# Optimization experiments

Hardware: AMD Instinct MI355X
Metric: run time of the kernel (lower is better)

## Reference

```python
import jax, jax.numpy as jnp
import numpy as np

B_, C_, T_, F_IN, H_, K_ = 64, 6, 128, 128, 128, 3


def _ln(x, g, b, eps=1e-5):
    # PyTorch LayerNorm: biased variance, eps=1e-5
    m = x.mean(-1, keepdims=True)
    v = ((x - m) ** 2).mean(-1, keepdims=True)
    return (x - m) / jnp.sqrt(v + eps) * g + b


def setup_inputs() -> dict:
    key = jax.random.key(0)
    ks = jax.random.split(key, 24)
    rn = lambda i, shape, s=1.0: jax.random.normal(ks[i], shape, jnp.float32) * s
    H = H_
    return dict(
        X_de=rn(0, (B_, C_, T_, F_IN)),
        # fe_proj: Linear(F_IN->H) + LayerNorm(H)
        W1=rn(1, (F_IN, H), 1.0 / np.sqrt(F_IN)), b1=rn(2, (H,), 0.02),
        ln1_g=1.0 + rn(3, (H,), 0.1), ln1_b=rn(4, (H,), 0.1),
        # LearnAdjacency: weight vector, scalar bias, LayerNorm(1)
        aw=rn(5, (H,), 0.1), ab=rn(6, (1,), 0.1),
        aln_g=1.0 + rn(7, (1,), 0.1), aln_b=rn(8, (1,), 0.1),
        # ChebConv: weights (K,H,H), bias (H), LayerNorm(H)
        cheb_w=rn(9, (K_, H, H), 1.0 / np.sqrt(H)), cheb_b=rn(10, (H,), 0.02),
        cln_g=1.0 + rn(11, (H,), 0.1), cln_b=rn(12, (H,), 0.1),
        # satt: Linear(2H->H) + LayerNorm(H) + Linear(H->1)
        sW1=rn(13, (2 * H, H), 1.0 / np.sqrt(2 * H)), sb1=rn(14, (H,), 0.02),
        sln_g=1.0 + rn(15, (H,), 0.1), sln_b=rn(16, (H,), 0.1),
        sW2=rn(17, (H, 1), 1.0 / np.sqrt(H)), sb2=rn(18, (1,), 0.02),
    )


def reference(X_de, W1, b1, ln1_g, ln1_b, aw, ab, aln_g, aln_b,
              cheb_w, cheb_b, cln_g, cln_b,
              sW1, sb1, sln_g, sln_b, sW2, sb2):
    b, C, T, Fin = X_de.shape
    H = W1.shape[1]
    K = cheb_w.shape[0]
    # fe_proj over every (b,t,c) node feature vector (Dropout = identity in eval)
    x = X_de.transpose(0, 2, 1, 3).reshape(b * T * C, Fin)  # (bTC, Fin)
    xn = jax.nn.gelu(_ln(x @ W1 + b1, ln1_g, ln1_b), approximate=False)
    Xn = xn.reshape(b, T, C, H)
    Xf = xn.reshape(b * T, C, H)  # fold T into batch; timesteps are independent
    # LearnAdjacency: pairwise |diff| -> scalar logit -> relu -> LayerNorm(1) -> row_softmax
    diff = jnp.abs(Xf[:, :, None, :] - Xf[:, None, :, :])  # (bT, C, C, H)
    logits = jax.nn.relu(jnp.einsum('bnjf,f->bnj', diff, aw) + ab)
    logits = _ln(logits[..., None], aln_g, aln_b)[..., 0]
    # row_softmax with eps=1e-8 in denominator (as in source)
    e = jnp.exp(logits - logits.max(-1, keepdims=True))
    adj = e / (e.sum(-1, keepdims=True) + 1e-8)  # (bT, C, C)
    # ChebConv with row-normalized A_hat = adj + I
    A_hat = adj + jnp.eye(C, dtype=adj.dtype)
    P = A_hat / jnp.maximum(A_hat.sum(-1, keepdims=True), 1e-6)
    out = jnp.einsum('bnf,fo->bno', Xf, cheb_w[0])
    Pk = Xf
    for k in range(1, K):  # K=3, static Chebyshev recurrence
        Pk = jnp.einsum('bnm,bmf->bnf', P, Pk)
        out = out + jnp.einsum('bnf,fo->bno', Pk, cheb_w[k])
    g = _ln(out + cheb_b, cln_g, cln_b)  # (bT, C, H); DropPath = identity in eval
    # attention gating
    nmean = jnp.einsum('bnm,bmf->bnf', adj, g)
    cat = jnp.concatenate([g, nmean], axis=-1)  # (bT, C, 2H)
    h = jax.nn.gelu(_ln(cat @ sW1 + sb1, sln_g, sln_b), approximate=False)
    att = jax.nn.sigmoid((h @ sW2 + sb2)[..., 0])[..., None]  # (bT, C, 1)
    epoch = (g * att).mean(axis=1)  # mean over nodes -> (bT, H)
    return (epoch.reshape(b, T, H),
            adj.reshape(b, T, C, C),
            Xn,
            g.reshape(b, T, C, H))
```

## Files before the change

### kernel.cpp

```cpp
#include <hip/hip_runtime.h>
#include <math.h>

typedef unsigned short u16;
typedef unsigned int u32;
typedef __attribute__((ext_vector_type(2))) float f32x2;
typedef __attribute__((ext_vector_type(4))) float f32x4;
typedef __attribute__((ext_vector_type(8))) short bf16x8;
typedef __attribute__((ext_vector_type(4))) u32 u32x4;

#define U_CONST   0.16666666638888889f
#define C1_CONST  0.5000000004166667f
#define C2_CONST  0.2500000004166667f
#define A_CONST   0.08333333326388889f
#define A1C_CONST 0.12499999993055555f

__device__ __forceinline__ float bf2f(u16 u){ union{u32 i; float f;} v; v.i=((u32)u)<<16; return v.f; }
__device__ __forceinline__ u16 f2bf(float f){ union{float f; u32 i;} v; v.f=f; u32 x=v.i;
  return (u16)((x + 0x7FFFu + ((x>>16)&1u)) >> 16); }

__device__ __forceinline__ u32 cvtpk(float lo, float hi){
  u32 r; asm("v_cvt_pk_bf16_f32 %0, %1, %2" : "=v"(r) : "v"(lo), "v"(hi)); return r;
}

__device__ __forceinline__ float gelu_f(float x){
  float ax = fabsf(x) * 0.7071067811865476f;
  float t  = __builtin_amdgcn_rcpf(fmaf(0.3275911f, ax, 1.0f));
  float p  = t*fmaf(t, fmaf(t, fmaf(t, fmaf(t, 1.061405429f, -1.453152027f),
                                    1.421413741f), -0.284496736f), 0.254829592f);
  float er = fmaf(-p, __expf(-ax*ax), 1.0f);
  er = copysignf(er, x);
  return 0.5f*x*(1.0f+er);
}
__device__ __forceinline__ float sigmoid_f(float z){
  return __builtin_amdgcn_rcpf(1.0f + __expf(-z));
}

__device__ __forceinline__ bf16x8 pack8(f32x4 a, f32x4 b){
  union { bf16x8 v; u32 w[4]; } r;
  r.w[0]=cvtpk(a[0],a[1]); r.w[1]=cvtpk(a[2],a[3]);
  r.w[2]=cvtpk(b[0],b[1]); r.w[3]=cvtpk(b[2],b[3]);
  return r.v;
}

template<bool GELU>
__device__ __forceinline__ void ln_rows(f32x4 (&acc)[8], const float* __restrict__ gvec,
                                        const float* __restrict__ bvec, int cl){
  float sm[4]={0,0,0,0}, sq[4]={0,0,0,0};
  #pragma unroll
  for (int n=0;n<8;n++)
    #pragma unroll
    for (int j=0;j<4;j++){ float x = acc[n][j]; sm[j]+=x; sq[j]+=x*x; }
  #pragma unroll
  for (int j=0;j<4;j++){
    #pragma unroll
    for (int off=1; off<16; off<<=1){ sm[j]+=__shfl_xor(sm[j],off); sq[j]+=__shfl_xor(sq[j],off); }
    float m = sm[j]*0.0078125f;
    float r = rsqrtf(sq[j]*0.0078125f - m*m + 1e-5f);
    sm[j]=m; sq[j]=r;
  }
  #pragma unroll
  for (int n=0;n<8;n++){
    float gg = gvec[(n<<4)+cl], be = bvec[(n<<4)+cl];
    #pragma unroll
    for (int j=0;j<4;j++){
      float y = (acc[n][j]-sm[j])*sq[j]*gg + be;
      acc[n][j] = GELU ? gelu_f(y) : y;
    }
  }
}

__device__ __forceinline__ void add_vec(f32x4 (&acc)[8], const float* __restrict__ v, int cl){
  #pragma unroll
  for (int n=0;n<8;n++){ float bv = v[(n<<4)+cl];
    #pragma unroll
    for (int j=0;j<4;j++) acc[n][j]+=bv; }
}

__device__ __forceinline__ void gsum(const f32x4 (&acc)[8], float (&s0)[8], float (&s1)[8], int cq){
  #pragma unroll
  for (int n=0;n<8;n++){
    float a=0.f, b=0.f;
    #pragma unroll
    for (int j=0;j<4;j++){
      int row = (cq<<2)+j;
      float y = acc[n][j];
      a += (row<6)? y : 0.f;
      b += (row>=6 && row<12)? y : 0.f;
    }
    a += __shfl_xor(a,16); a += __shfl_xor(a,32);
    b += __shfl_xor(b,16); b += __shfl_xor(b,32);
    s0[n]=a; s1[n]=b;
  }
}

__device__ __forceinline__ void spill(const f32x4 (&acc)[8], float* __restrict__ gdst,
                                      char* Al, int cl, int cq){
  #pragma unroll
  for (int n=0;n<8;n++)
    #pragma unroll
    for (int j=0;j<4;j++){
      int R=(cq<<2)+j;
      float y=acc[n][j], yo=__shfl_xor(y,1);
      if (R<12 && !(cl&1)){
        int col=(n<<4)+cl;
        *(f32x2*)(gdst + (size_t)R*128 + col) = (f32x2){y,yo};
        *(u32*)(Al + (R<<8) + ((col<<1) ^ ((R&7)<<4))) = cvtpk(y,yo);
      }
    }
}

__device__ __forceinline__ void ssave(const f32x4 (&acc)[8], char* Sl, int cl, int cq){
  float s0[8], s1[8];
  gsum(acc, s0, s1, cq);
  #pragma unroll
  for (int n=0;n<8;n++){
    float a_ = __shfl_xor(s0[n],1), b_ = __shfl_xor(s1[n],1);
    if (cq==0 && !(cl&1)){
      int col=(n<<4)+cl;
      *(u32*)(Sl + (col<<1))       = cvtpk(s0[n], a_);
      *(u32*)(Sl + 256 + (col<<1)) = cvtpk(s1[n], b_);
    }
  }
}

__device__ __forceinline__ void stageW(u16* Wb, const u16* __restrict__ slot, int tid){
  const u32x4* src = (const u32x4*)slot;
  #pragma unroll
  for (int it=0; it<4; ++it){
    int i = tid + (it<<9);
    int h = i >> 4, s = i & 15;
    u32x4 v = src[i];
    *(u32x4*)((char*)Wb + (h<<8) + ((s ^ (h&7))<<4)) = v;
  }
}
__device__ __forceinline__ bf16x8 bfrag(const u16* Wb, int col, int kt, int cq){
  int s = (kt<<2) + cq;
  return *(const bf16x8*)((const char*)Wb + (col<<8) + ((s ^ (col&7))<<4));
}
__device__ __forceinline__ bf16x8 afrag(const char* Al, int rl, int kt, int cq){
  return *(const bf16x8*)(Al + (rl<<8) + (((kt<<6)+(cq<<4)) ^ ((rl&7)<<4)));
}

template<bool INIT>
__device__ __forceinline__ void gemm_a(const u16* Wb, const char* Al, int rl, int cl, int cq,
                                       f32x4 (&acc)[8]){
  if (INIT){
    #pragma unroll
    for (int n=0;n<8;n++) acc[n]=(f32x4){0,0,0,0};
  }
  #pragma unroll
  for (int kt=0;kt<4;kt++){
    bf16x8 a = afrag(Al, rl, kt, cq);
    #pragma unroll
    for (int n=0;n<8;n++)
      acc[n] = __builtin_amdgcn_mfma_f32_16x16x32_bf16(a, bfrag(Wb,(n<<4)+cl,kt,cq), acc[n],0,0,0);
  }
}
__device__ __forceinline__ void gemm_s(const u16* Wb, const char* Sl, int grp, int cl, int cq,
                                       f32x4 (&acc)[8]){
  #pragma unroll
  for (int kt=0;kt<4;kt++){
    bf16x8 a = *(const bf16x8*)(Sl + (grp<<8) + (kt<<6) + (cq<<4));
    #pragma unroll
    for (int n=0;n<8;n++)
      acc[n] = __builtin_amdgcn_mfma_f32_16x16x32_bf16(a, bfrag(Wb,(n<<4)+cl,kt,cq), acc[n],0,0,0);
  }
}

__global__ void k_prep(const float* __restrict__ W1, const float* __restrict__ chw,
                       const float* __restrict__ sW1, u16* __restrict__ WT5){
  int i = blockIdx.x*256 + threadIdx.x;
  int dst = ((i&127)<<7) + (i>>7);
  float w0 = chw[i], w1 = chw[16384+i], w2 = chw[32768+i];
  WT5[dst]         = f2bf(W1[i]);
  WT5[16384+dst]   = f2bf(w0 + C1_CONST*w1 + C2_CONST*w2);
  WT5[32768+dst]   = f2bf(A_CONST*w1 + A1C_CONST*w2);
  WT5[49152+dst]   = f2bf(sW1[i]);
  WT5[65536+dst]   = f2bf(U_CONST*sW1[16384+i]);
}

__global__ __launch_bounds__(512, 4)
void k_all(const float* __restrict__ X_de, const u16* __restrict__ WT5,
           const float* __restrict__ b1, const float* __restrict__ ln1g, const float* __restrict__ ln1b,
           const float* __restrict__ chb, const float* __restrict__ clng, const float* __restrict__ clnb,
           const float* __restrict__ sb1, const float* __restrict__ slng, const float* __restrict__ slnb,
           const float* __restrict__ sW2, const float* __restrict__ sb2p,
           float* __restrict__ out)
{
  __shared__ __align__(16) u16  Wb[128*128];
  __shared__ __align__(16) char lds[8][3584];
  const int tid=threadIdx.x, w=tid>>6, lane=tid&63, cl=lane&15, cq=lane>>4;
  char* Al = lds[w];
  char* Sl = lds[w] + 3072;
  const int wid = blockIdx.x*8 + w;
  const int R0 = wid*12, g0 = wid*2;
  const int rl = (cl<12)? cl : 0;
  const int grp = (rl>=6)? 1 : 0;

  {
    float* adj = out + 1048576;
    #pragma unroll
    for (int k=0;k<2;k++){ int idx = tid + (k<<9); if (idx < 576) adj[(size_t)blockIdx.x*576 + idx] = 0.16666667f; }
  }

  int grow = R0 + rl;
  u32 grp6 = ((u32)grow * 43691u) >> 18;
  int c = grow - (int)grp6*6;
  const float* xrow = X_de + (((size_t)(((int)(grp6>>7))*6 + c)<<7) + (int)(grp6&127))*128 + (cq<<3);
  f32x4 xlo0 = *(const f32x4*)(xrow);
  f32x4 xhi0 = *(const f32x4*)(xrow+4);
  f32x4 xlo1 = *(const f32x4*)(xrow+32);
  f32x4 xhi1 = *(const f32x4*)(xrow+36);
  f32x4 xlo2 = *(const f32x4*)(xrow+64);
  f32x4 xhi2 = *(const f32x4*)(xrow+68);
  f32x4 xlo3 = *(const f32x4*)(xrow+96);
  f32x4 xhi3 = *(const f32x4*)(xrow+100);
  stageW(Wb, WT5, tid);
  bf16x8 af0 = pack8(xlo0,xhi0), af1 = pack8(xlo1,xhi1), af2 = pack8(xlo2,xhi2), af3 = pack8(xlo3,xhi3);
  __syncthreads();

  f32x4 acc[8];
  #pragma unroll
  for (int n=0;n<8;n++) acc[n]=(f32x4){0,0,0,0};
  #pragma unroll
  for (int n=0;n<8;n++) acc[n]=__builtin_amdgcn_mfma_f32_16x16x32_bf16(af0, bfrag(Wb,(n<<4)+cl,0,cq), acc[n],0,0,0);
  #pragma unroll
  for (int n=0;n<8;n++) acc[n]=__builtin_amdgcn_mfma_f32_16x16x32_bf16(af1, bfrag(Wb,(n<<4)+cl,1,cq), acc[n],0,0,0);
  #pragma unroll
  for (int n=0;n<8;n++) acc[n]=__builtin_amdgcn_mfma_f32_16x16x32_bf16(af2, bfrag(Wb,(n<<4)+cl,2,cq), acc[n],0,0,0);
  #pragma unroll
  for (int n=0;n<8;n++) acc[n]=__builtin_amdgcn_mfma_f32_16x16x32_bf16(af3, bfrag(Wb,(n<<4)+cl,3,cq), acc[n],0,0,0);
  add_vec(acc, b1, cl);
  ln_rows<true>(acc, ln1g, ln1b, cl);
  spill(acc, out + 1343488 + (size_t)R0*128, Al, cl, cq);
  ssave(acc, Sl, cl, cq);
  __syncthreads();

  stageW(Wb, WT5+16384, tid);
  __syncthreads();
  gemm_a<true>(Wb, Al, rl, cl, cq, acc);
  __syncthreads();
  stageW(Wb, WT5+32768, tid);
  __syncthreads();
  gemm_s(Wb, Sl, grp, cl, cq, acc);
  add_vec(acc, chb, cl);
  ln_rows<false>(acc, clng, clnb, cl);
  spill(acc, out + 7634944 + (size_t)R0*128, Al, cl, cq);
  ssave(acc, Sl, cl, cq);
  __syncthreads();

  stageW(Wb, WT5+49152, tid);
  __syncthreads();
  gemm_a<true>(Wb, Al, rl, cl, cq, acc);
  __syncthreads();
  stageW(Wb, WT5+65536, tid);
  __syncthreads();
  gemm_s(Wb, Sl, grp, cl, cq, acc);
  add_vec(acc, sb1, cl);
  ln_rows<true>(acc, slng, slnb, cl);

  float z0=0,z1=0,z2=0,z3=0;
  #pragma unroll
  for (int n=0;n<8;n++){
    float wv = sW2[(n<<4)+cl];
    z0 = fmaf(acc[n][0], wv, z0); z1 = fmaf(acc[n][1], wv, z1);
    z2 = fmaf(acc[n][2], wv, z2); z3 = fmaf(acc[n][3], wv, z3);
  }
  #pragma unroll
  for (int off=1; off<16; off<<=1){
    z0 += __shfl_xor(z0,off); z1 += __shfl_xor(z1,off);
    z2 += __shfl_xor(z2,off); z3 += __shfl_xor(z3,off);
  }
  float s2 = sb2p[0];
  float a0 = sigmoid_f(z0+s2), a1 = sigmoid_f(z1+s2), a2 = sigmoid_f(z2+s2), a3 = sigmoid_f(z3+s2);

  float attr[12];
  #pragma unroll
  for (int r=0;r<12;r++){
    int src = (r>>2)<<4;
    float v = (r&3)==0 ? a0 : (r&3)==1 ? a1 : (r&3)==2 ? a2 : a3;
    attr[r] = __shfl(v, src);
  }
  const int c2 = lane<<1;
  #pragma unroll
  for (int gi=0; gi<2; ++gi){
    float ex=0.f, ey=0.f;
    #pragma unroll
    for (int i=0;i<6;i++){
      int r = gi*6+i;
      u32 p = *(const u32*)(Al + (r<<8) + ((c2<<1) ^ ((r&7)<<4)));
      ex = fmaf(attr[r], bf2f((u16)(p&0xFFFFu)), ex);
      ey = fmaf(attr[r], bf2f((u16)(p>>16)), ey);
    }
    *(f32x2*)(out + (size_t)(g0+gi)*128 + c2) = (f32x2){ex*(1.0f/6.0f), ey*(1.0f/6.0f)};
  }
}

extern "C" void kernel_launch(void* const* d_in, const int* in_sizes, int n_in,
                              void* d_out, int out_size, void* d_ws, size_t ws_size,
                              hipStream_t stream){
  const float* X_de = (const float*)d_in[0];
  const float* W1   = (const float*)d_in[1];
  const float* b1   = (const float*)d_in[2];
  const float* ln1g = (const float*)d_in[3];
  const float* ln1b = (const float*)d_in[4];
  const float* chw  = (const float*)d_in[9];
  const float* chb  = (const float*)d_in[10];
  const float* clng = (const float*)d_in[11];
  const float* clnb = (const float*)d_in[12];
  const float* sW1  = (const float*)d_in[13];
  const float* sb1  = (const float*)d_in[14];
  const float* slng = (const float*)d_in[15];
  const float* slnb = (const float*)d_in[16];
  const float* sW2  = (const float*)d_in[17];
  const float* sb2  = (const float*)d_in[18];

  float* out = (float*)d_out;
  u16* WT5 = (u16*)d_ws;

  hipLaunchKernelGGL(k_prep, dim3(64),  dim3(256), 0, stream, W1, chw, sW1, WT5);
  hipLaunchKernelGGL(k_all,  dim3(512), dim3(512), 0, stream,
                     X_de, WT5, b1, ln1g, ln1b, chb, clng, clnb,
                     sb1, slng, slnb, sW2, sb2, out);
}
```

Baseline: 53.96 us.

## Prefetch next weight slice into registers and use DPP for lane reductions

```diff
diff --git a/kernel.cpp b/kernel.cpp
--- a/kernel.cpp
+++ b/kernel.cpp
@@ -20,6 +20,17 @@
 
 __device__ __forceinline__ u32 cvtpk(float lo, float hi){
   u32 r; asm("v_cvt_pk_bf16_f32 %0, %1, %2" : "=v"(r) : "v"(lo), "v"(hi)); return r;
+}
+
+template<int C> __device__ __forceinline__ float dpp_mov(float x){
+  return __int_as_float(__builtin_amdgcn_update_dpp(0, __float_as_int(x), C, 0xF, 0xF, true));
+}
+__device__ __forceinline__ float dpp_sum16(float v){
+  v += dpp_mov<0xB1>(v);
+  v += dpp_mov<0x4E>(v);
+  v += dpp_mov<0x141>(v);
+  v += dpp_mov<0x140>(v);
+  return v;
 }
 
 __device__ __forceinline__ float gelu_f(float x){
@@ -52,8 +63,8 @@
     for (int j=0;j<4;j++){ float x = acc[n][j]; sm[j]+=x; sq[j]+=x*x; }
   #pragma unroll
   for (int j=0;j<4;j++){
-    #pragma unroll
-    for (int off=1; off<16; off<<=1){ sm[j]+=__shfl_xor(sm[j],off); sq[j]+=__shfl_xor(sq[j],off); }
+    sm[j] = dpp_sum16(sm[j]);
+    sq[j] = dpp_sum16(sq[j]);
     float m = sm[j]*0.0078125f;
     float r = rsqrtf(sq[j]*0.0078125f - m*m + 1e-5f);
     sm[j]=m; sq[j]=r;
@@ -100,7 +111,8 @@
     #pragma unroll
     for (int j=0;j<4;j++){
       int R=(cq<<2)+j;
-      float y=acc[n][j], yo=__shfl_xor(y,1);
+      float y=acc[n][j];
+      float yo=dpp_mov<0xB1>(y);
       if (R<12 && !(cl&1)){
         int col=(n<<4)+cl;
         *(f32x2*)(gdst + (size_t)R*128 + col) = (f32x2){y,yo};
@@ -114,7 +126,7 @@
   gsum(acc, s0, s1, cq);
   #pragma unroll
   for (int n=0;n<8;n++){
-    float a_ = __shfl_xor(s0[n],1), b_ = __shfl_xor(s1[n],1);
+    float a_ = dpp_mov<0xB1>(s0[n]), b_ = dpp_mov<0xB1>(s1[n]);
     if (cq==0 && !(cl&1)){
       int col=(n<<4)+cl;
       *(u32*)(Sl + (col<<1))       = cvtpk(s0[n], a_);
@@ -123,14 +135,16 @@
   }
 }
 
-__device__ __forceinline__ void stageW(u16* Wb, const u16* __restrict__ slot, int tid){
-  const u32x4* src = (const u32x4*)slot;
+__device__ __forceinline__ void wload(u32x4 (&wp)[4], const u16* __restrict__ slot, int tid){
+  const u32x4* s = (const u32x4*)slot;
+  wp[0]=s[tid]; wp[1]=s[tid+512]; wp[2]=s[tid+1024]; wp[3]=s[tid+1536];
+}
+__device__ __forceinline__ void wwrite(u16* Wb, const u32x4 (&wp)[4], int tid){
   #pragma unroll
   for (int it=0; it<4; ++it){
     int i = tid + (it<<9);
     int h = i >> 4, s = i & 15;
-    u32x4 v = src[i];
-    *(u32x4*)((char*)Wb + (h<<8) + ((s ^ (h&7))<<4)) = v;
+    *(u32x4*)((char*)Wb + (h<<8) + ((s ^ (h&7))<<4)) = wp[it];
   }
 }
 __device__ __forceinline__ bf16x8 bfrag(const u16* Wb, int col, int kt, int cq){
@@ -197,6 +211,8 @@
   const int rl = (cl<12)? cl : 0;
   const int grp = (rl>=6)? 1 : 0;
 
+  u32x4 wp[4];
+
   {
     float* adj = out + 1048576;
     #pragma unroll
@@ -215,9 +231,11 @@
   f32x4 xhi2 = *(const f32x4*)(xrow+68);
   f32x4 xlo3 = *(const f32x4*)(xrow+96);
   f32x4 xhi3 = *(const f32x4*)(xrow+100);
-  stageW(Wb, WT5, tid);
+  wload(wp, WT5, tid);
+  wwrite(Wb, wp, tid);
   bf16x8 af0 = pack8(xlo0,xhi0), af1 = pack8(xlo1,xhi1), af2 = pack8(xlo2,xhi2), af3 = pack8(xlo3,xhi3);
   __syncthreads();
+  wload(wp, WT5+16384, tid);
 
   f32x4 acc[8];
   #pragma unroll
@@ -235,25 +253,28 @@
   spill(acc, out + 1343488 + (size_t)R0*128, Al, cl, cq);
   ssave(acc, Sl, cl, cq);
   __syncthreads();
-
-  stageW(Wb, WT5+16384, tid);
-  __syncthreads();
+  wwrite(Wb, wp, tid);
+  __syncthreads();
+  wload(wp, WT5+32768, tid);
+
   gemm_a<true>(Wb, Al, rl, cl, cq, acc);
   __syncthreads();
-  stageW(Wb, WT5+32768, tid);
-  __syncthreads();
+  wwrite(Wb, wp, tid);
+  __syncthreads();
+  wload(wp, WT5+49152, tid);
   gemm_s(Wb, Sl, grp, cl, cq, acc);
   add_vec(acc, chb, cl);
   ln_rows<false>(acc, clng, clnb, cl);
   spill(acc, out + 7634944 + (size_t)R0*128, Al, cl, cq);
   ssave(acc, Sl, cl, cq);
   __syncthreads();
-
-  stageW(Wb, WT5+49152, tid);
-  __syncthreads();
+  wwrite(Wb, wp, tid);
+  __syncthreads();
+  wload(wp, WT5+65536, tid);
+
   gemm_a<true>(Wb, Al, rl, cl, cq, acc);
   __syncthreads();
-  stageW(Wb, WT5+65536, tid);
+  wwrite(Wb, wp, tid);
   __syncthreads();
   gemm_s(Wb, Sl, grp, cl, cq, acc);
   add_vec(acc, sb1, cl);
@@ -266,11 +287,7 @@
     z0 = fmaf(acc[n][0], wv, z0); z1 = fmaf(acc[n][1], wv, z1);
     z2 = fmaf(acc[n][2], wv, z2); z3 = fmaf(acc[n][3], wv, z3);
   }
-  #pragma unroll
-  for (int off=1; off<16; off<<=1){
-    z0 += __shfl_xor(z0,off); z1 += __shfl_xor(z1,off);
-    z2 += __shfl_xor(z2,off); z3 += __shfl_xor(z3,off);
-  }
+  z0 = dpp_sum16(z0); z1 = dpp_sum16(z1); z2 = dpp_sum16(z2); z3 = dpp_sum16(z3);
   float s2 = sb2p[0];
   float a0 = sigmoid_f(z0+s2), a1 = sigmoid_f(z1+s2), a2 = sigmoid_f(z2+s2), a3 = sigmoid_f(z3+s2);
 
```

Measured after the change: 71.48 us. 32.5% more time.
